# Kernel tuning notes

Hardware: AMD Instinct MI355X
Metric: run time of the kernel (lower is better)

The kernel has to match this reference:

```python
import jax, jax.numpy as jnp
import numpy as np

B, NQ, NC, D, H, RBH = 2, 512, 2048, 768, 8, 64
HD = D // H
FFN = 4 * D
EPS = 1e-5


def _ln(x, g, b):
    m = jnp.mean(x, axis=-1, keepdims=True)
    v = jnp.mean((x - m) ** 2, axis=-1, keepdims=True)
    return (x - m) * jax.lax.rsqrt(v + EPS) * g + b


def _heads(x):  # (B,N,D) -> (B,H,N,HD)
    return x.reshape(x.shape[0], x.shape[1], H, HD).transpose(0, 2, 1, 3)


def _merge(x):  # (B,H,N,HD) -> (B,N,D)
    return x.transpose(0, 2, 1, 3).reshape(x.shape[0], x.shape[2], D)


def _attn(q, k, v, bias=None):
    logits = jnp.einsum('bhqd,bhkd->bhqk', q, k) * (HD ** -0.5)
    if bias is not None:
        logits = logits + bias
    a = jax.nn.softmax(logits, axis=-1)
    return jnp.einsum('bhqk,bhkd->bhqd', a, v)


def setup_inputs() -> dict:
    key = jax.random.key(0)
    ks = jax.random.split(key, 40)
    s = 0.02
    inp = {
        'query_state': jax.random.normal(ks[0], (B, NQ, D), jnp.float32),
        'context_k': jax.random.normal(ks[1], (B, NC, D), jnp.float32),
        'context_v': jax.random.normal(ks[2], (B, NC, D), jnp.float32),
        'query_coords': jax.random.uniform(ks[3], (B, NQ, 2), jnp.float32),
        'context_coords': jax.random.uniform(ks[4], (B, NC, 2), jnp.float32),
        'sn_g': jnp.ones((D,), jnp.float32), 'sn_b': jnp.zeros((D,), jnp.float32),
        'sa_wq': jax.random.normal(ks[5], (D, D)) * s, 'sa_bq': jnp.zeros((D,)),
        'sa_wk': jax.random.normal(ks[6], (D, D)) * s, 'sa_bk': jnp.zeros((D,)),
        'sa_wv': jax.random.normal(ks[7], (D, D)) * s, 'sa_bv': jnp.zeros((D,)),
        'sa_wo': jax.random.normal(ks[8], (D, D)) * s, 'sa_bo': jnp.zeros((D,)),
        'cn_g': jnp.ones((D,), jnp.float32), 'cn_b': jnp.zeros((D,), jnp.float32),
        'ca_wq': jax.random.normal(ks[9], (D, D)) * s, 'ca_bq': jnp.zeros((D,)),
        'ca_wk': jax.random.normal(ks[10], (D, D)) * s, 'ca_bk': jnp.zeros((D,)),
        'ca_wv': jax.random.normal(ks[11], (D, D)) * s, 'ca_bv': jnp.zeros((D,)),
        'ca_wo': jax.random.normal(ks[12], (D, D)) * s, 'ca_bo': jnp.zeros((D,)),
        'rb_w1': jax.random.normal(ks[13], (2, RBH)) * 0.5, 'rb_b1': jnp.zeros((RBH,)),
        'rb_w2': jax.random.normal(ks[14], (RBH, H)) * 0.1, 'rb_b2': jnp.zeros((H,)),
        'fn_g': jnp.ones((D,), jnp.float32), 'fn_b': jnp.zeros((D,), jnp.float32),
        'ffn_w1': jax.random.normal(ks[15], (D, FFN)) * s, 'ffn_b1': jnp.zeros((FFN,)),
        'ffn_w2': jax.random.normal(ks[16], (FFN, D)) * s, 'ffn_b2': jnp.zeros((D,)),
    }
    return {k2: jnp.asarray(v, jnp.float32) for k2, v in inp.items()}


def reference(query_state, context_k, context_v, query_coords, context_coords,
              sn_g, sn_b, sa_wq, sa_bq, sa_wk, sa_bk, sa_wv, sa_bv, sa_wo, sa_bo,
              cn_g, cn_b, ca_wq, ca_bq, ca_wk, ca_bk, ca_wv, ca_bv, ca_wo, ca_bo,
              rb_w1, rb_b1, rb_w2, rb_b2,
              fn_g, fn_b, ffn_w1, ffn_b1, ffn_w2, ffn_b2):
    # --- self-attention (pre-norm) ---
    qn = _ln(query_state, sn_g, sn_b)
    q = _heads(qn @ sa_wq + sa_bq)
    k = _heads(qn @ sa_wk + sa_bk)
    v = _heads(qn @ sa_wv + sa_bv)
    self_out = _merge(_attn(q, k, v)) @ sa_wo + sa_bo
    x = query_state + self_out
    # --- relative coordinate bias: (B,Nq,Nc,2) -> (B,H,Nq,Nc) ---
    delta = query_coords[:, :, None, :] - context_coords[:, None, :, :]
    h = jax.nn.gelu(delta @ rb_w1 + rb_b1, approximate=False)
    bias = (h @ rb_w2 + rb_b2).transpose(0, 3, 1, 2)
    # --- cross-attention with bias ---
    qn = _ln(x, cn_g, cn_b)
    q = _heads(qn @ ca_wq + ca_bq)
    k = _heads(context_k @ ca_wk + ca_bk)
    v = _heads(context_v @ ca_wv + ca_bv)
    cross_out = _merge(_attn(q, k, v, bias)) @ ca_wo + ca_bo
    x = x + cross_out
    # --- FFN ---
    hn = _ln(x, fn_g, fn_b)
    ffn_out = jax.nn.gelu(hn @ ffn_w1 + ffn_b1, approximate=False) @ ffn_w2 + ffn_b2
    return x + ffn_out
```

## Files before the change

kernel.cpp:

```cpp
#include <hip/hip_runtime.h>
#include <hip/hip_bf16.h>

typedef __bf16 bf16x8 __attribute__((ext_vector_type(8)));
typedef float  f32x4  __attribute__((ext_vector_type(4)));
typedef float  f32x2  __attribute__((ext_vector_type(2)));
typedef __hip_bfloat16 bf16_t;

constexpr int CB  = 2;
constexpr int CNQ = 512;
constexpr int CNC = 2048;
constexpr int CD  = 768;
constexpr int CH  = 8;
constexpr int CHD = 96;
constexpr int CFFN = 3072;

static __device__ __forceinline__ float gelu_f(float x) {
    float x2 = x * x;
    float zn = x * fmaf(x2, -0.07135481f, -1.5957692f);
    float e  = __expf(zn);
    return x * __builtin_amdgcn_rcpf(1.0f + e);
}

__global__ __launch_bounds__(256) void ln_kernel(const float* __restrict__ x,
                                                 const float* __restrict__ g,
                                                 const float* __restrict__ b,
                                                 bf16_t* __restrict__ out) {
    __shared__ float red[8];
    long row = blockIdx.x;
    const float* xr = x + row * CD;
    int t = threadIdx.x;
    float v0 = xr[t], v1 = xr[t + 256], v2 = xr[t + 512];
    float s  = v0 + v1 + v2;
    float sq = v0 * v0 + v1 * v1 + v2 * v2;
    #pragma unroll
    for (int o = 32; o; o >>= 1) { s += __shfl_xor(s, o); sq += __shfl_xor(sq, o); }
    if ((t & 63) == 0) { red[t >> 6] = s; red[4 + (t >> 6)] = sq; }
    __syncthreads();
    s  = red[0] + red[1] + red[2] + red[3];
    sq = red[4] + red[5] + red[6] + red[7];
    float mean = s * (1.0f / 768.0f);
    float var  = sq * (1.0f / 768.0f) - mean * mean;
    float inv  = rsqrtf(var + 1e-5f);
    bf16_t* orow = out + row * CD;
    orow[t]       = __float2bfloat16((v0 - mean) * inv * g[t]       + b[t]);
    orow[t + 256] = __float2bfloat16((v1 - mean) * inv * g[t + 256] + b[t + 256]);
    orow[t + 512] = __float2bfloat16((v2 - mean) * inv * g[t + 512] + b[t + 512]);
}

__global__ __launch_bounds__(256) void cvt_kernel(const float* __restrict__ in,
                                                  bf16_t* __restrict__ out, long n) {
    long i = ((long)blockIdx.x * 256 + threadIdx.x) * 4;
    float4 v = *(const float4*)&in[i];
    out[i]     = __float2bfloat16(v.x);
    out[i + 1] = __float2bfloat16(v.y);
    out[i + 2] = __float2bfloat16(v.z);
    out[i + 3] = __float2bfloat16(v.w);
}

__global__ __launch_bounds__(256) void wtrans_kernel(const float* __restrict__ W,
                                                     bf16_t* __restrict__ Wt, int K, int N) {
    __shared__ float tile[32][33];
    int tx = threadIdx.x & 31, ty = threadIdx.x >> 5;
    int bx = blockIdx.x, by = blockIdx.y;
    #pragma unroll
    for (int i = 0; i < 4; ++i) {
        int k = by * 32 + ty + i * 8;
        tile[ty + i * 8][tx] = W[(long)k * N + bx * 32 + tx];
    }
    __syncthreads();
    #pragma unroll
    for (int i = 0; i < 4; ++i) {
        int n = bx * 32 + ty + i * 8;
        Wt[(long)n * K + by * 32 + tx] = __float2bfloat16(tile[tx][ty + i * 8]);
    }
}

__global__ __launch_bounds__(256) void relbias_kernel(const float* __restrict__ qc,
                                                      const float* __restrict__ cc,
                                                      const float* __restrict__ w1,
                                                      const float* __restrict__ b1,
                                                      const float* __restrict__ w2,
                                                      const float* __restrict__ b2,
                                                      bf16_t* __restrict__ bias) {
    long idx = (long)blockIdx.x * 256 + threadIdx.x;
    int  kk = (int)(idx & (CNC - 1));
    long t2 = idx >> 11;
    int  q  = (int)(t2 & (CNQ - 1));
    int  b  = (int)(t2 >> 9);
    float d0 = qc[((long)b * CNQ + q) * 2]     - cc[((long)b * CNC + kk) * 2];
    float d1 = qc[((long)b * CNQ + q) * 2 + 1] - cc[((long)b * CNC + kk) * 2 + 1];
    f32x2 acc[4];
    #pragma unroll
    for (int i = 0; i < 4; ++i) { acc[i][0] = b2[2 * i]; acc[i][1] = b2[2 * i + 1]; }
    #pragma unroll 8
    for (int j = 0; j < 64; ++j) {
        float x = fmaf(d0, w1[j], fmaf(d1, w1[64 + j], b1[j]));
        float x2 = x * x;
        float zn = x * fmaf(x2, -0.07135481f, -1.5957692f);
        float e  = __expf(zn);
        float h  = x * __builtin_amdgcn_rcpf(1.0f + e);
        f32x2 hv = {h, h};
        const f32x2* w2r = (const f32x2*)&w2[j * CH];
        #pragma unroll
        for (int i = 0; i < 4; ++i) acc[i] += hv * w2r[i];
    }
    long qk = (long)q * CNC + kk;
    #pragma unroll
    for (int hh = 0; hh < CH; ++hh)
        bias[(long)(b * CH + hh) * CNQ * CNC + qk] = __float2bfloat16(acc[hh >> 1][hh & 1]);
}

template<int NPT>
__global__ __launch_bounds__(256) void softmax_kernel(float* __restrict__ S, long ld) {
    __shared__ float red[8];
    long row = blockIdx.x;
    float* base = S + row * ld;
    int t = threadIdx.x;
    const int c0 = t * NPT;
    float v[NPT];
    #pragma unroll
    for (int i = 0; i < NPT; ++i) v[i] = base[c0 + i];
    float m = v[0];
    #pragma unroll
    for (int i = 1; i < NPT; ++i) m = fmaxf(m, v[i]);
    #pragma unroll
    for (int o = 32; o; o >>= 1) m = fmaxf(m, __shfl_xor(m, o));
    if ((t & 63) == 0) red[t >> 6] = m;
    __syncthreads();
    m = fmaxf(fmaxf(red[0], red[1]), fmaxf(red[2], red[3]));
    float s = 0.0f;
    #pragma unroll
    for (int i = 0; i < NPT; ++i) { v[i] = __expf(v[i] - m); s += v[i]; }
    #pragma unroll
    for (int o = 32; o; o >>= 1) s += __shfl_xor(s, o);
    __syncthreads();
    if ((t & 63) == 0) red[4 + (t >> 6)] = s;
    __syncthreads();
    s = red[4] + red[5] + red[6] + red[7];
    float inv = 1.0f / s;
    bf16_t* ob = (bf16_t*)base;
    #pragma unroll
    for (int i = 0; i < NPT; ++i) ob[c0 + i] = __float2bfloat16(v[i] * inv);
}

template<int MF, int NF, int BK, int OUT, bool BIAS, bool B2D, bool GELU_E, bool RES>
__global__ __launch_bounds__(256) void gemm_nt(
        const bf16_t* __restrict__ A, long ldA, long zsA,
        const bf16_t* __restrict__ Bt, long ldB, long zsB,
        const float* __restrict__ bias,
        const bf16_t* __restrict__ b2d, long zs2d, long ld2d,
        const float* __restrict__ res,
        void* __restrict__ Cout, long ldC, long zsC,
        int K, int NR, float scale) {
    constexpr int BM = MF * 32, BN = NF * 32;
    constexpr int PAD = 4, LDT = BK + PAD;
    constexpr int SEGS = BK / 8;
    static_assert((BM * SEGS) % 256 == 0 && (BN * SEGS) % 256 == 0, "staging divisibility");
    __shared__ __bf16 As[BM * LDT];
    __shared__ __bf16 Bs[BN * LDT];
    const int tid = threadIdx.x;
    const int z = blockIdx.z;
    const int m0 = blockIdx.y * BM, n0 = blockIdx.x * BN;
    const bf16_t* Ab = A + (long)z * zsA + (long)m0 * ldA;
    const bf16_t* Bb = Bt + (long)z * zsB + (long)n0 * ldB;
    const int w = tid >> 6, lane = tid & 63;
    const int wm = w >> 1, wn = w & 1;
    const int l15 = lane & 15, l4 = lane >> 4;
    f32x4 acc[MF][NF] = {};
    for (int k0 = 0; k0 < K; k0 += BK) {
        #pragma unroll
        for (int it = 0; it < (BM * SEGS) / 256; ++it) {
            int c = tid + it * 256;
            int r = c / SEGS, sg = c % SEGS;
            *(bf16x8*)&As[r * LDT + sg * 8] = *(const bf16x8*)&Ab[(long)r * ldA + k0 + sg * 8];
        }
        #pragma unroll
        for (int it = 0; it < (BN * SEGS) / 256; ++it) {
            int c = tid + it * 256;
            int r = c / SEGS, sg = c % SEGS;
            *(bf16x8*)&Bs[r * LDT + sg * 8] = *(const bf16x8*)&Bb[(long)r * ldB + k0 + sg * 8];
        }
        __syncthreads();
        #pragma unroll
        for (int s = 0; s < BK / 32; ++s) {
            bf16x8 af[MF], bfr[NF];
            #pragma unroll
            for (int i = 0; i < MF; ++i)
                af[i] = *(const bf16x8*)&As[(wm * MF * 16 + i * 16 + l15) * LDT + s * 32 + l4 * 8];
            #pragma unroll
            for (int j = 0; j < NF; ++j)
                bfr[j] = *(const bf16x8*)&Bs[(wn * NF * 16 + j * 16 + l15) * LDT + s * 32 + l4 * 8];
            #pragma unroll
            for (int i = 0; i < MF; ++i)
                #pragma unroll
                for (int j = 0; j < NF; ++j)
                    acc[i][j] = __builtin_amdgcn_mfma_f32_16x16x32_bf16(af[i], bfr[j], acc[i][j], 0, 0, 0);
        }
        __syncthreads();
    }
    #pragma unroll
    for (int i = 0; i < MF; ++i) {
        const int rbase = m0 + wm * MF * 16 + i * 16 + l4 * 4;
        #pragma unroll
        for (int j = 0; j < NF; ++j) {
            const int col = n0 + wn * NF * 16 + j * 16 + l15;
            #pragma unroll
            for (int r = 0; r < 4; ++r) {
                int row = rbase + r;
                float v = acc[i][j][r] * scale;
                if constexpr (BIAS) v += bias[col];
                if constexpr (B2D)  v += __bfloat162float(b2d[(long)z * zs2d + (long)row * ld2d + col]);
                if constexpr (GELU_E) v = gelu_f(v);
                if constexpr (RES)  v += res[(long)row * ldC + col];
                if constexpr (OUT == 0) {
                    ((float*)Cout)[(long)z * zsC + (long)row * ldC + col] = v;
                } else if constexpr (OUT == 1) {
                    ((bf16_t*)Cout)[(long)z * zsC + (long)row * ldC + col] = __float2bfloat16(v);
                } else if constexpr (OUT == 2) {
                    int bb = row / NR, n = row - bb * NR;
                    int hh = col / CHD, dd = col - hh * CHD;
                    ((bf16_t*)Cout)[((long)(bb * CH + hh) * NR + n) * CHD + dd] = __float2bfloat16(v);
                } else if constexpr (OUT == 3) {
                    int bb = row / NR, n = row - bb * NR;
                    int hh = col / CHD, dd = col - hh * CHD;
                    ((bf16_t*)Cout)[((long)(bb * CH + hh) * CHD + dd) * NR + n] = __float2bfloat16(v);
                } else {
                    int bb = z / CH, hh = z - bb * CH;
                    ((bf16_t*)Cout)[((long)bb * CNQ + row) * CD + hh * CHD + col] = __float2bfloat16(v);
                }
            }
        }
    }
}

extern "C" void kernel_launch(void* const* d_in, const int* in_sizes, int n_in,
                              void* d_out, int out_size, void* d_ws, size_t ws_size,
                              hipStream_t stream) {
    const float* query_state    = (const float*)d_in[0];
    const float* context_k      = (const float*)d_in[1];
    const float* context_v      = (const float*)d_in[2];
    const float* query_coords   = (const float*)d_in[3];
    const float* context_coords = (const float*)d_in[4];
    const float* sn_g = (const float*)d_in[5];  const float* sn_b = (const float*)d_in[6];
    const float* sa_wq = (const float*)d_in[7];  const float* sa_bq = (const float*)d_in[8];
    const float* sa_wk = (const float*)d_in[9];  const float* sa_bk = (const float*)d_in[10];
    const float* sa_wv = (const float*)d_in[11]; const float* sa_bv = (const float*)d_in[12];
    const float* sa_wo = (const float*)d_in[13]; const float* sa_bo = (const float*)d_in[14];
    const float* cn_g = (const float*)d_in[15];  const float* cn_b = (const float*)d_in[16];
    const float* ca_wq = (const float*)d_in[17]; const float* ca_bq = (const float*)d_in[18];
    const float* ca_wk = (const float*)d_in[19]; const float* ca_bk = (const float*)d_in[20];
    const float* ca_wv = (const float*)d_in[21]; const float* ca_bv = (const float*)d_in[22];
    const float* ca_wo = (const float*)d_in[23]; const float* ca_bo = (const float*)d_in[24];
    const float* rb_w1 = (const float*)d_in[25]; const float* rb_b1 = (const float*)d_in[26];
    const float* rb_w2 = (const float*)d_in[27]; const float* rb_b2 = (const float*)d_in[28];
    const float* fn_g = (const float*)d_in[29];  const float* fn_b = (const float*)d_in[30];
    const float* ffn_w1 = (const float*)d_in[31]; const float* ffn_b1 = (const float*)d_in[32];
    const float* ffn_w2 = (const float*)d_in[33]; const float* ffn_b2 = (const float*)d_in[34];
    float* out = (float*)d_out;

    char* p = (char*)d_ws;
    auto alloc = [&](size_t bytes) -> char* {
        char* r = p; p += (bytes + 255) & ~(size_t)255; return r;
    };
    const size_t WDD = (size_t)CD * CD, WDF = (size_t)CD * CFFN;
    bf16_t* sa_wq_t = (bf16_t*)alloc(WDD * 2);
    bf16_t* sa_wk_t = (bf16_t*)alloc(WDD * 2);
    bf16_t* sa_wv_t = (bf16_t*)alloc(WDD * 2);
    bf16_t* sa_wo_t = (bf16_t*)alloc(WDD * 2);
    bf16_t* ca_wq_t = (bf16_t*)alloc(WDD * 2);
    bf16_t* ca_wk_t = (bf16_t*)alloc(WDD * 2);
    bf16_t* ca_wv_t = (bf16_t*)alloc(WDD * 2);
    bf16_t* ca_wo_t = (bf16_t*)alloc(WDD * 2);
    bf16_t* ffn_w1_t = (bf16_t*)alloc(WDF * 2);
    bf16_t* ffn_w2_t = (bf16_t*)alloc(WDF * 2);
    bf16_t* ln_buf   = (bf16_t*)alloc((size_t)CB * CNQ * CD * 2);
    bf16_t* q_split  = (bf16_t*)alloc((size_t)CB * CH * CNQ * CHD * 2);
    bf16_t* k_split  = (bf16_t*)alloc((size_t)CB * CH * CNQ * CHD * 2);
    bf16_t* v_splitT = (bf16_t*)alloc((size_t)CB * CH * CNQ * CHD * 2);
    bf16_t* ck_b     = (bf16_t*)alloc((size_t)CB * CNC * CD * 2);
    bf16_t* cv_b     = (bf16_t*)alloc((size_t)CB * CNC * CD * 2);
    bf16_t* kc_split = (bf16_t*)alloc((size_t)CB * CH * CNC * CHD * 2);
    bf16_t* vc_splitT= (bf16_t*)alloc((size_t)CB * CH * CNC * CHD * 2);
    float*  S        = (float*)alloc((size_t)CB * CH * CNQ * CNC * 4);
    bf16_t* bias2d   = (bf16_t*)alloc((size_t)CB * CH * CNQ * CNC * 2);
    bf16_t* attn_m   = (bf16_t*)alloc((size_t)CB * CNQ * CD * 2);
    float*  xbuf     = (float*)alloc((size_t)CB * CNQ * CD * 4);
    bf16_t* ffn_h    = (bf16_t*)alloc((size_t)CB * CNQ * CFFN * 2);

    const dim3 tb(256);
    const float qk_scale = 0.10206207261596575f;

    wtrans_kernel<<<dim3(CD / 32, CD / 32), tb, 0, stream>>>(sa_wq, sa_wq_t, CD, CD);
    wtrans_kernel<<<dim3(CD / 32, CD / 32), tb, 0, stream>>>(sa_wk, sa_wk_t, CD, CD);
    wtrans_kernel<<<dim3(CD / 32, CD / 32), tb, 0, stream>>>(sa_wv, sa_wv_t, CD, CD);
    wtrans_kernel<<<dim3(CD / 32, CD / 32), tb, 0, stream>>>(sa_wo, sa_wo_t, CD, CD);
    wtrans_kernel<<<dim3(CD / 32, CD / 32), tb, 0, stream>>>(ca_wq, ca_wq_t, CD, CD);
    wtrans_kernel<<<dim3(CD / 32, CD / 32), tb, 0, stream>>>(ca_wk, ca_wk_t, CD, CD);
    wtrans_kernel<<<dim3(CD / 32, CD / 32), tb, 0, stream>>>(ca_wv, ca_wv_t, CD, CD);
    wtrans_kernel<<<dim3(CD / 32, CD / 32), tb, 0, stream>>>(ca_wo, ca_wo_t, CD, CD);
    wtrans_kernel<<<dim3(CFFN / 32, CD / 32), tb, 0, stream>>>(ffn_w1, ffn_w1_t, CD, CFFN);
    wtrans_kernel<<<dim3(CD / 32, CFFN / 32), tb, 0, stream>>>(ffn_w2, ffn_w2_t, CFFN, CD);
    cvt_kernel<<<(CB * CNC * CD) / 1024, tb, 0, stream>>>(context_k, ck_b, (long)CB * CNC * CD);
    cvt_kernel<<<(CB * CNC * CD) / 1024, tb, 0, stream>>>(context_v, cv_b, (long)CB * CNC * CD);
    relbias_kernel<<<(CB * CNQ * CNC) / 256, tb, 0, stream>>>(query_coords, context_coords,
                                                              rb_w1, rb_b1, rb_w2, rb_b2, bias2d);
    ln_kernel<<<CB * CNQ, tb, 0, stream>>>(query_state, sn_g, sn_b, ln_buf);
    gemm_nt<2,2,64,2,true,false,false,false><<<dim3(CD / 64, (CB * CNQ) / 64, 1), tb, 0, stream>>>(
        ln_buf, CD, 0, sa_wq_t, CD, 0, sa_bq, nullptr, 0, 0, nullptr, q_split, 0, 0, CD, CNQ, 1.0f);
    gemm_nt<2,2,64,2,true,false,false,false><<<dim3(CD / 64, (CB * CNQ) / 64, 1), tb, 0, stream>>>(
        ln_buf, CD, 0, sa_wk_t, CD, 0, sa_bk, nullptr, 0, 0, nullptr, k_split, 0, 0, CD, CNQ, 1.0f);
    gemm_nt<2,2,64,3,true,false,false,false><<<dim3(CD / 64, (CB * CNQ) / 64, 1), tb, 0, stream>>>(
        ln_buf, CD, 0, sa_wv_t, CD, 0, sa_bv, nullptr, 0, 0, nullptr, v_splitT, 0, 0, CD, CNQ, 1.0f);
    gemm_nt<4,2,96,0,false,false,false,false><<<dim3(CNQ / 64, CNQ / 128, CB * CH), tb, 0, stream>>>(
        q_split, CHD, (long)CNQ * CHD, k_split, CHD, (long)CNQ * CHD,
        nullptr, nullptr, 0, 0, nullptr, S, CNQ, (long)CNQ * CNQ, CHD, 0, qk_scale);
    softmax_kernel<2><<<CB * CH * CNQ, tb, 0, stream>>>(S, CNQ);
    gemm_nt<2,3,64,4,false,false,false,false><<<dim3(1, CNQ / 64, CB * CH), tb, 0, stream>>>(
        (const bf16_t*)S, 2 * CNQ, (long)CNQ * 2 * CNQ, v_splitT, CNQ, (long)CHD * CNQ,
        nullptr, nullptr, 0, 0, nullptr, attn_m, 0, 0, CNQ, CNQ, 1.0f);
    gemm_nt<2,2,64,0,true,false,false,true><<<dim3(CD / 64, (CB * CNQ) / 64, 1), tb, 0, stream>>>(
        attn_m, CD, 0, sa_wo_t, CD, 0, sa_bo, nullptr, 0, 0, query_state, xbuf, CD, 0, CD, 0, 1.0f);
    ln_kernel<<<CB * CNQ, tb, 0, stream>>>(xbuf, cn_g, cn_b, ln_buf);
    gemm_nt<2,2,64,2,true,false,false,false><<<dim3(CD / 64, (CB * CNQ) / 64, 1), tb, 0, stream>>>(
        ln_buf, CD, 0, ca_wq_t, CD, 0, ca_bq, nullptr, 0, 0, nullptr, q_split, 0, 0, CD, CNQ, 1.0f);
    gemm_nt<4,4,64,2,true,false,false,false><<<dim3(CD / 128, (CB * CNC) / 128, 1), tb, 0, stream>>>(
        ck_b, CD, 0, ca_wk_t, CD, 0, ca_bk, nullptr, 0, 0, nullptr, kc_split, 0, 0, CD, CNC, 1.0f);
    gemm_nt<4,4,64,3,true,false,false,false><<<dim3(CD / 128, (CB * CNC) / 128, 1), tb, 0, stream>>>(
        cv_b, CD, 0, ca_wv_t, CD, 0, ca_bv, nullptr, 0, 0, nullptr, vc_splitT, 0, 0, CD, CNC, 1.0f);
    gemm_nt<4,2,96,0,false,true,false,false><<<dim3(CNC / 64, CNQ / 128, CB * CH), tb, 0, stream>>>(
        q_split, CHD, (long)CNQ * CHD, kc_split, CHD, (long)CNC * CHD,
        nullptr, bias2d, (long)CNQ * CNC, CNC, nullptr, S, CNC, (long)CNQ * CNC, CHD, 0, qk_scale);
    softmax_kernel<8><<<CB * CH * CNQ, tb, 0, stream>>>(S, CNC);
    gemm_nt<2,3,64,4,false,false,false,false><<<dim3(1, CNQ / 64, CB * CH), tb, 0, stream>>>(
        (const bf16_t*)S, 2 * CNC, (long)CNQ * 2 * CNC, vc_splitT, CNC, (long)CHD * CNC,
        nullptr, nullptr, 0, 0, nullptr, attn_m, 0, 0, CNC, CNQ, 1.0f);
    gemm_nt<2,2,64,0,true,false,false,true><<<dim3(CD / 64, (CB * CNQ) / 64, 1), tb, 0, stream>>>(
        attn_m, CD, 0, ca_wo_t, CD, 0, ca_bo, nullptr, 0, 0, xbuf, xbuf, CD, 0, CD, 0, 1.0f);
    ln_kernel<<<CB * CNQ, tb, 0, stream>>>(xbuf, fn_g, fn_b, ln_buf);
    gemm_nt<4,4,64,1,true,false,true,false><<<dim3(CFFN / 128, (CB * CNQ) / 128, 1), tb, 0, stream>>>(
        ln_buf, CD, 0, ffn_w1_t, CD, 0, ffn_b1, nullptr, 0, 0, nullptr, ffn_h, CFFN, 0, CD, 0, 1.0f);
    gemm_nt<2,2,64,0,true,false,false,true><<<dim3(CD / 64, (CB * CNQ) / 64, 1), tb, 0, stream>>>(
        ffn_h, CFFN, 0, ffn_w2_t, CFFN, 0, ffn_b2, nullptr, 0, 0, xbuf, out, CD, 0, CFFN, 0, 1.0f);
}
```

Before: 516.2 us.

## Fuse QKV projection, batch weight transposes, convert context inside GEMM

Concatenates the self-attention Q/K/V weights and biases so a single GEMM with a split-scatter epilogue produces all three head-split outputs. The eight DxD weight transposes become one batched launch. The separate fp32-to-bf16 conversion of context_k/v is removed by letting the GEMM load fp32 A tiles and convert them while staging. Several tile shapes also change (smaller M tiles for PV, 128x64 tiles for context and FFN1) to raise block counts. These cut launch count and an extra round trip through memory, but per-element branching in the epilogue and fp32 loads of A are added costs.

```diff
diff --git a/kernel.cpp b/kernel.cpp
--- a/kernel.cpp
+++ b/kernel.cpp
@@ -47,14 +47,25 @@
     orow[t + 512] = __float2bfloat16((v2 - mean) * inv * g[t + 512] + b[t + 512]);
 }
 
-__global__ __launch_bounds__(256) void cvt_kernel(const float* __restrict__ in,
-                                                  bf16_t* __restrict__ out, long n) {
-    long i = ((long)blockIdx.x * 256 + threadIdx.x) * 4;
-    float4 v = *(const float4*)&in[i];
-    out[i]     = __float2bfloat16(v.x);
-    out[i + 1] = __float2bfloat16(v.y);
-    out[i + 2] = __float2bfloat16(v.z);
-    out[i + 3] = __float2bfloat16(v.w);
+__global__ __launch_bounds__(256) void wtrans8_kernel(
+        const float* W0, const float* W1, const float* W2, const float* W3,
+        const float* W4, const float* W5, const float* W6, const float* W7,
+        bf16_t* T0, bf16_t* T1, bf16_t* T2, bf16_t* T3,
+        bf16_t* T4, bf16_t* T5, bf16_t* T6, bf16_t* T7) {
+    const float* Ws[8] = {W0, W1, W2, W3, W4, W5, W6, W7};
+    bf16_t*      Ts[8] = {T0, T1, T2, T3, T4, T5, T6, T7};
+    const float* W = Ws[blockIdx.z];
+    bf16_t*      T = Ts[blockIdx.z];
+    __shared__ float tile[32][33];
+    int tx = threadIdx.x & 31, ty = threadIdx.x >> 5;
+    int bx = blockIdx.x, by = blockIdx.y;
+    #pragma unroll
+    for (int i = 0; i < 4; ++i)
+        tile[ty + i * 8][tx] = W[(long)(by * 32 + ty + i * 8) * CD + bx * 32 + tx];
+    __syncthreads();
+    #pragma unroll
+    for (int i = 0; i < 4; ++i)
+        T[(long)(bx * 32 + ty + i * 8) * CD + by * 32 + tx] = __float2bfloat16(tile[tx][ty + i * 8]);
 }
 
 __global__ __launch_bounds__(256) void wtrans_kernel(const float* __restrict__ W,
@@ -73,6 +84,15 @@
         int n = bx * 32 + ty + i * 8;
         Wt[(long)n * K + by * 32 + tx] = __float2bfloat16(tile[tx][ty + i * 8]);
     }
+}
+
+__global__ __launch_bounds__(256) void biascat_kernel(const float* __restrict__ b0,
+                                                      const float* __restrict__ b1,
+                                                      const float* __restrict__ b2,
+                                                      float* __restrict__ out) {
+    int i = blockIdx.x * 256 + threadIdx.x;
+    float v = i < 768 ? b0[i] : (i < 1536 ? b1[i - 768] : b2[i - 1536]);
+    out[i] = v;
 }
 
 __global__ __launch_bounds__(256) void relbias_kernel(const float* __restrict__ qc,
@@ -143,9 +163,9 @@
     for (int i = 0; i < NPT; ++i) ob[c0 + i] = __float2bfloat16(v[i] * inv);
 }
 
-template<int MF, int NF, int BK, int OUT, bool BIAS, bool B2D, bool GELU_E, bool RES>
+template<int MF, int NF, int BK, int OUT, bool BIAS, bool B2D, bool GELU_E, bool RES, bool AF32 = false>
 __global__ __launch_bounds__(256) void gemm_nt(
-        const bf16_t* __restrict__ A, long ldA, long zsA,
+        const void* __restrict__ Araw, long ldA, long zsA,
         const bf16_t* __restrict__ Bt, long ldB, long zsB,
         const float* __restrict__ bias,
         const bf16_t* __restrict__ b2d, long zs2d, long ld2d,
@@ -155,24 +175,42 @@
     constexpr int BM = MF * 32, BN = NF * 32;
     constexpr int PAD = 4, LDT = BK + PAD;
     constexpr int SEGS = BK / 8;
-    static_assert((BM * SEGS) % 256 == 0 && (BN * SEGS) % 256 == 0, "staging divisibility");
+    static_assert((BN * SEGS) % 256 == 0, "B staging divisibility");
     __shared__ __bf16 As[BM * LDT];
     __shared__ __bf16 Bs[BN * LDT];
     const int tid = threadIdx.x;
     const int z = blockIdx.z;
     const int m0 = blockIdx.y * BM, n0 = blockIdx.x * BN;
-    const bf16_t* Ab = A + (long)z * zsA + (long)m0 * ldA;
+    const bf16_t* Ab = nullptr; const float* Af = nullptr;
+    if constexpr (AF32) Af = (const float*)Araw + (long)z * zsA + (long)m0 * ldA;
+    else                Ab = (const bf16_t*)Araw + (long)z * zsA + (long)m0 * ldA;
     const bf16_t* Bb = Bt + (long)z * zsB + (long)n0 * ldB;
     const int w = tid >> 6, lane = tid & 63;
     const int wm = w >> 1, wn = w & 1;
     const int l15 = lane & 15, l4 = lane >> 4;
     f32x4 acc[MF][NF] = {};
     for (int k0 = 0; k0 < K; k0 += BK) {
-        #pragma unroll
-        for (int it = 0; it < (BM * SEGS) / 256; ++it) {
-            int c = tid + it * 256;
-            int r = c / SEGS, sg = c % SEGS;
-            *(bf16x8*)&As[r * LDT + sg * 8] = *(const bf16x8*)&Ab[(long)r * ldA + k0 + sg * 8];
+        if constexpr (AF32) {
+            constexpr int SEGA = BK / 4;
+            static_assert((BM * SEGA) % 256 == 0, "A f32 staging divisibility");
+            #pragma unroll
+            for (int it = 0; it < (BM * SEGA) / 256; ++it) {
+                int c = tid + it * 256;
+                int r = c / SEGA, sg = c % SEGA;
+                float4 v = *(const float4*)&Af[(long)r * ldA + k0 + sg * 4];
+                union { bf16_t b[4]; uint2 u; } cv;
+                cv.b[0] = __float2bfloat16(v.x); cv.b[1] = __float2bfloat16(v.y);
+                cv.b[2] = __float2bfloat16(v.z); cv.b[3] = __float2bfloat16(v.w);
+                *(uint2*)&As[r * LDT + sg * 4] = cv.u;
+            }
+        } else {
+            static_assert((BM * SEGS) % 256 == 0 || AF32, "A staging divisibility");
+            #pragma unroll
+            for (int it = 0; it < (BM * SEGS) / 256; ++it) {
+                int c = tid + it * 256;
+                int r = c / SEGS, sg = c % SEGS;
+                *(bf16x8*)&As[r * LDT + sg * 8] = *(const bf16x8*)&Ab[(long)r * ldA + k0 + sg * 8];
+            }
         }
         #pragma unroll
         for (int it = 0; it < (BN * SEGS) / 256; ++it) {
@@ -224,9 +262,20 @@
                     int bb = row / NR, n = row - bb * NR;
                     int hh = col / CHD, dd = col - hh * CHD;
                     ((bf16_t*)Cout)[((long)(bb * CH + hh) * CHD + dd) * NR + n] = __float2bfloat16(v);
-                } else {
+                } else if constexpr (OUT == 4) {
                     int bb = z / CH, hh = z - bb * CH;
                     ((bf16_t*)Cout)[((long)bb * CNQ + row) * CD + hh * CHD + col] = __float2bfloat16(v);
+                } else {
+                    constexpr long QSZ5 = (long)CB * CH * CNQ * CHD;
+                    int part = col / CD;
+                    int c = col - part * CD;
+                    int hh = c / CHD, dd = c - hh * CHD;
+                    int bb = row / CNQ, n = row - bb * CNQ;
+                    long off;
+                    if (part == 0)      off = ((long)(bb * CH + hh) * CNQ + n) * CHD + dd;
+                    else if (part == 1) off = QSZ5 + ((long)(bb * CH + hh) * CNQ + n) * CHD + dd;
+                    else                off = 2 * QSZ5 + ((long)(bb * CH + hh) * CHD + dd) * CNQ + n;
+                    ((bf16_t*)Cout)[off] = __float2bfloat16(v);
                 }
             }
         }
@@ -263,9 +312,8 @@
         char* r = p; p += (bytes + 255) & ~(size_t)255; return r;
     };
     const size_t WDD = (size_t)CD * CD, WDF = (size_t)CD * CFFN;
-    bf16_t* sa_wq_t = (bf16_t*)alloc(WDD * 2);
-    bf16_t* sa_wk_t = (bf16_t*)alloc(WDD * 2);
-    bf16_t* sa_wv_t = (bf16_t*)alloc(WDD * 2);
+    const size_t QSZ = (size_t)CB * CH * CNQ * CHD;
+    bf16_t* qkv_wt  = (bf16_t*)alloc(3 * WDD * 2);
     bf16_t* sa_wo_t = (bf16_t*)alloc(WDD * 2);
     bf16_t* ca_wq_t = (bf16_t*)alloc(WDD * 2);
     bf16_t* ca_wk_t = (bf16_t*)alloc(WDD * 2);
@@ -273,12 +321,9 @@
     bf16_t* ca_wo_t = (bf16_t*)alloc(WDD * 2);
     bf16_t* ffn_w1_t = (bf16_t*)alloc(WDF * 2);
     bf16_t* ffn_w2_t = (bf16_t*)alloc(WDF * 2);
+    float*  qkv_bias = (float*)alloc(2304 * 4);
     bf16_t* ln_buf   = (bf16_t*)alloc((size_t)CB * CNQ * CD * 2);
-    bf16_t* q_split  = (bf16_t*)alloc((size_t)CB * CH * CNQ * CHD * 2);
-    bf16_t* k_split  = (bf16_t*)alloc((size_t)CB * CH * CNQ * CHD * 2);
-    bf16_t* v_splitT = (bf16_t*)alloc((size_t)CB * CH * CNQ * CHD * 2);
-    bf16_t* ck_b     = (bf16_t*)alloc((size_t)CB * CNC * CD * 2);
-    bf16_t* cv_b     = (bf16_t*)alloc((size_t)CB * CNC * CD * 2);
+    bf16_t* qkvs     = (bf16_t*)alloc(3 * QSZ * 2);
     bf16_t* kc_split = (bf16_t*)alloc((size_t)CB * CH * CNC * CHD * 2);
     bf16_t* vc_splitT= (bf16_t*)alloc((size_t)CB * CH * CNC * CHD * 2);
     float*  S        = (float*)alloc((size_t)CB * CH * CNQ * CNC * 4);
@@ -286,36 +331,29 @@
     bf16_t* attn_m   = (bf16_t*)alloc((size_t)CB * CNQ * CD * 2);
     float*  xbuf     = (float*)alloc((size_t)CB * CNQ * CD * 4);
     bf16_t* ffn_h    = (bf16_t*)alloc((size_t)CB * CNQ * CFFN * 2);
+    bf16_t* q_split  = qkvs;
+    bf16_t* k_split  = qkvs + QSZ;
+    bf16_t* v_splitT = qkvs + 2 * QSZ;
 
     const dim3 tb(256);
     const float qk_scale = 0.10206207261596575f;
 
-    wtrans_kernel<<<dim3(CD / 32, CD / 32), tb, 0, stream>>>(sa_wq, sa_wq_t, CD, CD);
-    wtrans_kernel<<<dim3(CD / 32, CD / 32), tb, 0, stream>>>(sa_wk, sa_wk_t, CD, CD);
-    wtrans_kernel<<<dim3(CD / 32, CD / 32), tb, 0, stream>>>(sa_wv, sa_wv_t, CD, CD);
-    wtrans_kernel<<<dim3(CD / 32, CD / 32), tb, 0, stream>>>(sa_wo, sa_wo_t, CD, CD);
-    wtrans_kernel<<<dim3(CD / 32, CD / 32), tb, 0, stream>>>(ca_wq, ca_wq_t, CD, CD);
-    wtrans_kernel<<<dim3(CD / 32, CD / 32), tb, 0, stream>>>(ca_wk, ca_wk_t, CD, CD);
-    wtrans_kernel<<<dim3(CD / 32, CD / 32), tb, 0, stream>>>(ca_wv, ca_wv_t, CD, CD);
-    wtrans_kernel<<<dim3(CD / 32, CD / 32), tb, 0, stream>>>(ca_wo, ca_wo_t, CD, CD);
+    wtrans8_kernel<<<dim3(CD / 32, CD / 32, 8), tb, 0, stream>>>(
+        sa_wq, sa_wk, sa_wv, sa_wo, ca_wq, ca_wk, ca_wv, ca_wo,
+        qkv_wt, qkv_wt + WDD, qkv_wt + 2 * WDD, sa_wo_t, ca_wq_t, ca_wk_t, ca_wv_t, ca_wo_t);
     wtrans_kernel<<<dim3(CFFN / 32, CD / 32), tb, 0, stream>>>(ffn_w1, ffn_w1_t, CD, CFFN);
     wtrans_kernel<<<dim3(CD / 32, CFFN / 32), tb, 0, stream>>>(ffn_w2, ffn_w2_t, CFFN, CD);
-    cvt_kernel<<<(CB * CNC * CD) / 1024, tb, 0, stream>>>(context_k, ck_b, (long)CB * CNC * CD);
-    cvt_kernel<<<(CB * CNC * CD) / 1024, tb, 0, stream>>>(context_v, cv_b, (long)CB * CNC * CD);
+    biascat_kernel<<<9, tb, 0, stream>>>(sa_bq, sa_bk, sa_bv, qkv_bias);
     relbias_kernel<<<(CB * CNQ * CNC) / 256, tb, 0, stream>>>(query_coords, context_coords,
                                                               rb_w1, rb_b1, rb_w2, rb_b2, bias2d);
     ln_kernel<<<CB * CNQ, tb, 0, stream>>>(query_state, sn_g, sn_b, ln_buf);
-    gemm_nt<2,2,64,2,true,false,false,false><<<dim3(CD / 64, (CB * CNQ) / 64, 1), tb, 0, stream>>>(
-        ln_buf, CD, 0, sa_wq_t, CD, 0, sa_bq, nullptr, 0, 0, nullptr, q_split, 0, 0, CD, CNQ, 1.0f);
-    gemm_nt<2,2,64,2,true,false,false,false><<<dim3(CD / 64, (CB * CNQ) / 64, 1), tb, 0, stream>>>(
-        ln_buf, CD, 0, sa_wk_t, CD, 0, sa_bk, nullptr, 0, 0, nullptr, k_split, 0, 0, CD, CNQ, 1.0f);
-    gemm_nt<2,2,64,3,true,false,false,false><<<dim3(CD / 64, (CB * CNQ) / 64, 1), tb, 0, stream>>>(
-        ln_buf, CD, 0, sa_wv_t, CD, 0, sa_bv, nullptr, 0, 0, nullptr, v_splitT, 0, 0, CD, CNQ, 1.0f);
+    gemm_nt<4,2,64,5,true,false,false,false><<<dim3(2304 / 64, (CB * CNQ) / 128, 1), tb, 0, stream>>>(
+        ln_buf, CD, 0, qkv_wt, CD, 0, qkv_bias, nullptr, 0, 0, nullptr, qkvs, 0, 0, CD, CNQ, 1.0f);
     gemm_nt<4,2,96,0,false,false,false,false><<<dim3(CNQ / 64, CNQ / 128, CB * CH), tb, 0, stream>>>(
         q_split, CHD, (long)CNQ * CHD, k_split, CHD, (long)CNQ * CHD,
         nullptr, nullptr, 0, 0, nullptr, S, CNQ, (long)CNQ * CNQ, CHD, 0, qk_scale);
     softmax_kernel<2><<<CB * CH * CNQ, tb, 0, stream>>>(S, CNQ);
-    gemm_nt<2,3,64,4,false,false,false,false><<<dim3(1, CNQ / 64, CB * CH), tb, 0, stream>>>(
+    gemm_nt<1,3,64,4,false,false,false,false><<<dim3(1, CNQ / 32, CB * CH), tb, 0, stream>>>(
         (const bf16_t*)S, 2 * CNQ, (long)CNQ * 2 * CNQ, v_splitT, CNQ, (long)CHD * CNQ,
         nullptr, nullptr, 0, 0, nullptr, attn_m, 0, 0, CNQ, CNQ, 1.0f);
     gemm_nt<2,2,64,0,true,false,false,true><<<dim3(CD / 64, (CB * CNQ) / 64, 1), tb, 0, stream>>>(
@@ -323,21 +361,21 @@
     ln_kernel<<<CB * CNQ, tb, 0, stream>>>(xbuf, cn_g, cn_b, ln_buf);
     gemm_nt<2,2,64,2,true,false,false,false><<<dim3(CD / 64, (CB * CNQ) / 64, 1), tb, 0, stream>>>(
         ln_buf, CD, 0, ca_wq_t, CD, 0, ca_bq, nullptr, 0, 0, nullptr, q_split, 0, 0, CD, CNQ, 1.0f);
-    gemm_nt<4,4,64,2,true,false,false,false><<<dim3(CD / 128, (CB * CNC) / 128, 1), tb, 0, stream>>>(
-        ck_b, CD, 0, ca_wk_t, CD, 0, ca_bk, nullptr, 0, 0, nullptr, kc_split, 0, 0, CD, CNC, 1.0f);
-    gemm_nt<4,4,64,3,true,false,false,false><<<dim3(CD / 128, (CB * CNC) / 128, 1), tb, 0, stream>>>(
-        cv_b, CD, 0, ca_wv_t, CD, 0, ca_bv, nullptr, 0, 0, nullptr, vc_splitT, 0, 0, CD, CNC, 1.0f);
+    gemm_nt<4,2,64,2,true,false,false,false,true><<<dim3(CD / 64, (CB * CNC) / 128, 1), tb, 0, stream>>>(
+        context_k, CD, 0, ca_wk_t, CD, 0, ca_bk, nullptr, 0, 0, nullptr, kc_split, 0, 0, CD, CNC, 1.0f);
+    gemm_nt<4,2,64,3,true,false,false,false,true><<<dim3(CD / 64, (CB * CNC) / 128, 1), tb, 0, stream>>>(
+        context_v, CD, 0, ca_wv_t, CD, 0, ca_bv, nullptr, 0, 0, nullptr, vc_splitT, 0, 0, CD, CNC, 1.0f);
     gemm_nt<4,2,96,0,false,true,false,false><<<dim3(CNC / 64, CNQ / 128, CB * CH), tb, 0, stream>>>(
         q_split, CHD, (long)CNQ * CHD, kc_split, CHD, (long)CNC * CHD,
         nullptr, bias2d, (long)CNQ * CNC, CNC, nullptr, S, CNC, (long)CNQ * CNC, CHD, 0, qk_scale);
     softmax_kernel<8><<<CB * CH * CNQ, tb, 0, stream>>>(S, CNC);
-    gemm_nt<2,3,64,4,false,false,false,false><<<dim3(1, CNQ / 64, CB * CH), tb, 0, stream>>>(
+    gemm_nt<1,3,64,4,false,false,false,false><<<dim3(1, CNQ / 32, CB * CH), tb, 0, stream>>>(
         (const bf16_t*)S, 2 * CNC, (long)CNQ * 2 * CNC, vc_splitT, CNC, (long)CHD * CNC,
         nullptr, nullptr, 0, 0, nullptr, attn_m, 0, 0, CNC, CNQ, 1.0f);
     gemm_nt<2,2,64,0,true,false,false,true><<<dim3(CD / 64, (CB * CNQ) / 64, 1), tb, 0, stream>>>(
         attn_m, CD, 0, ca_wo_t, CD, 0, ca_bo, nullptr, 0, 0, xbuf, xbuf, CD, 0, CD, 0, 1.0f);
     ln_kernel<<<CB * CNQ, tb, 0, stream>>>(xbuf, fn_g, fn_b, ln_buf);
-    gemm_nt<4,4,64,1,true,false,true,false><<<dim3(CFFN / 128, (CB * CNQ) / 128, 1), tb, 0, stream>>>(
+    gemm_nt<4,2,64,1,true,false,true,false><<<dim3(CFFN / 64, (CB * CNQ) / 128, 1), tb, 0, stream>>>(
         ln_buf, CD, 0, ffn_w1_t, CD, 0, ffn_b1, nullptr, 0, 0, nullptr, ffn_h, CFFN, 0, CD, 0, 1.0f);
     gemm_nt<2,2,64,0,true,false,false,true><<<dim3(CD / 64, (CB * CNQ) / 64, 1), tb, 0, stream>>>(
         ffn_h, CFFN, 0, ffn_w2_t, CFFN, 0, ffn_b2, nullptr, 0, 0, xbuf, out, CD, 0, CFFN, 0, 1.0f);
```

After: 485.8 us. -5.9%, faster.
